# Performance work log

Measured on AMD Instinct MI355X. Metric: run time of the kernel, lower is better.

Reference implementation:

```python
import jax, jax.numpy as jnp
import numpy as np

B, C, W, H = 16, 512, 64, 64
OUT, NH = 512, 8
HD = OUT // NH          # 64
K = 64                  # kernel_size == attended axis length (height)


def setup_inputs() -> dict:
    key = jax.random.key(0)
    k0, k1, k2, k3 = jax.random.split(key, 4)
    s = float(HD) ** -0.5
    return {
        "x": jax.random.normal(k0, (B, C, W, H), jnp.float32),
        "in_proj_weight": jax.random.normal(k1, (2 * OUT, C), jnp.float32) * s,
        "in_proj_bias": jnp.zeros((2 * OUT,), jnp.float32),
        "out_proj_w": jax.random.normal(k2, (OUT, OUT), jnp.float32) * s,
        "out_proj_b": jnp.zeros((OUT,), jnp.float32),
        "relative": jax.random.normal(k3, (2 * HD, 2 * K - 1), jnp.float32) * s,
    }


def reference(x, in_proj_weight, in_proj_bias, out_proj_w, out_proj_b, relative):
    b, c, w, h = x.shape
    hd2 = HD // 2
    # width=False, self-attention path: permute(0,3,2,1) then flat view
    xq = jnp.transpose(x, (0, 3, 2, 1)).reshape(b * w, h, c)
    qkv = xq @ in_proj_weight.T + in_proj_bias
    q, k, v = jnp.split(qkv, [OUT // 2, OUT], axis=2)

    # relative position embeddings gathered into [2*HD, K, K]
    rel_idx = jnp.arange(K)[:, None] - jnp.arange(K)[None, :] + (K - 1)  # key i, query j
    emb = relative[:, rel_idx]                                          # [2*HD, K, K]
    q_emb, k_emb, v_emb = jnp.split(emb, [hd2, HD], axis=0)

    # [bw, heads, ch, pos]
    q = q.reshape(b * w, h, NH, hd2).transpose(0, 2, 3, 1)
    k = k.reshape(b * w, h, NH, hd2).transpose(0, 2, 3, 1)
    v = v.reshape(b * w, h, NH, HD).transpose(0, 2, 3, 1)

    qr = jnp.einsum('bgci,cij->bgij', q, q_emb)
    kr = jnp.einsum('bgci,cij->bgij', k, k_emb).swapaxes(2, 3)
    qk = jnp.einsum('bgci,bgcj->bgij', q, k)
    sim = jax.nn.softmax(qk + qr + kr, axis=3)

    sv = jnp.einsum('bgij,bgcj->bgci', sim, v)     # [bw, NH, HD, h]
    sve = jnp.einsum('bgij,cij->bgci', sim, v_emb)  # [bw, NH, HD, h]
    out = (sv + sve).reshape(b * w, OUT, h).swapaxes(1, 2)  # [bw, h, OUT]
    out = out @ out_proj_w.T + out_proj_b
    # [b, w, h, OUT] -> transpose(2,3) -> permute(0,2,3,1) == transpose(0,3,2,1)
    out = out.reshape(b, w, h, OUT).transpose(0, 3, 2, 1)   # [B, OUT, H, W]
    return out
```

## Files before the change

### kernel.cpp

```cpp
#include <hip/hip_runtime.h>

using u16 = unsigned short;
using u32 = unsigned int;
typedef __attribute__((ext_vector_type(8))) _Float16 h8v;
typedef __attribute__((ext_vector_type(8))) u16 us8;
typedef __attribute__((ext_vector_type(2))) u32 u32x2;
typedef __attribute__((ext_vector_type(4))) float f4v;

__device__ __forceinline__ u16 f2h(float f) {
  _Float16 h = (_Float16)f;
  return __builtin_bit_cast(unsigned short, h);
}
__device__ __forceinline__ _Float16 bits2h(u16 u) {
  return __builtin_bit_cast(_Float16, u);
}

__device__ __forceinline__ f4v mfma16(h8v a, h8v b, f4v c) {
  return __builtin_amdgcn_mfma_f32_16x16x32_f16(a, b, c, 0, 0, 0);
}

__device__ __forceinline__ void gll16(const void* g, void* l) {
  __builtin_amdgcn_global_load_lds(
      (const __attribute__((address_space(1))) void*)g,
      (__attribute__((address_space(3))) void*)l, 16, 0, 0);
}


__global__ __launch_bounds__(256) void k0_setup(
    const float* __restrict__ w1, const float* __restrict__ wout,
    const float* __restrict__ rel, u16* __restrict__ W1b, u16* __restrict__ Woutb,
    u16* __restrict__ EqT, u16* __restrict__ EkT, u16* __restrict__ Evp)
{
  int idx = blockIdx.x * 256 + threadIdx.x;
  if (idx < 524288) {
    W1b[idx] = f2h(w1[idx]);
  } else if (idx < 786432) {
    int k = idx - 524288; Woutb[k] = f2h(wout[k]);
  } else if (idx < 790528) {
    int k = idx - 786432; int t = k >> 5, c = k & 31;
    EqT[k] = (t < 127) ? f2h(rel[c * 127 + t]) : (u16)0;
  } else if (idx < 794624) {
    int k = idx - 790528; int t = k >> 5, c = k & 31;
    EkT[k] = (t < 127) ? f2h(rel[(32 + c) * 127 + t]) : (u16)0;
  } else if (idx < 802816) {
    int k = idx - 794624; int c = k >> 7, t = k & 127;
    Evp[k] = (t < 127) ? f2h(rel[(64 + c) * 127 + t]) : (u16)0;
  }
}

__global__ __launch_bounds__(256) void k0t_transpose(
    const float* __restrict__ x, u16* __restrict__ xT)
{
  const int bid = blockIdx.x;
  const int cc = bid & 7, w = (bid >> 3) & 63, b = bid >> 9;
  const int c0 = cc * 64;
  const int t = threadIdx.x;
  __shared__ float T[64 * 65];

  const float* xb = x + ((size_t)(b * 512 + c0) * 64 + w) * 64;
#pragma unroll
  for (int p = 0; p < 4; p++) {
    int ci = (t >> 4) + p * 16;
    int pos = (t & 15) * 4;
    float4 v = *(const float4*)&xb[(size_t)ci * 4096 + pos];
    T[ci * 65 + pos + 0] = v.x; T[ci * 65 + pos + 1] = v.y;
    T[ci * 65 + pos + 2] = v.z; T[ci * 65 + pos + 3] = v.w;
  }
  __syncthreads();
  size_t Rb = (size_t)b * 4096 + (size_t)w * 64;
#pragma unroll
  for (int p = 0; p < 2; p++) {
    int u = p * 256 + t;
    int h = u >> 3, ch = u & 7;
    us8 o;
#pragma unroll
    for (int e = 0; e < 8; e++) o[e] = f2h(T[(ch * 8 + e) * 65 + h]);
    *(us8*)&xT[(Rb + h) * 512 + c0 + ch * 8] = o;
  }
}

__global__ __launch_bounds__(512, 1) void k1_qkv(
    const u16* __restrict__ xT, const u16* __restrict__ W1b,
    const float* __restrict__ bias, u16* __restrict__ qkv)
{
  __shared__ u16 POOL[81920];
  u16* XL = POOL;
  u16* Bl = POOL + 65536;
  const int rt = blockIdx.x;
  const int b = rt >> 5, w0 = (rt & 31) * 2;
  const int tid = threadIdx.x;
  const int l = tid & 63, wv = tid >> 6;
  const int lr = l & 15, lg = l >> 4;
  const int osub = (wv & 1) * 64;
  const int rsub = (wv >> 1) * 32;
  const size_t Rbase = (size_t)rt * 128;

#pragma unroll
  for (int i = 0; i < 16; i++) {
    int r = wv * 16 + i;
    gll16(xT + (Rbase + r) * 512 + ((l ^ (r & 7)) << 3), XL + r * 512);
  }

  auto stageB = [&](int ot, int kk, int buf) {
#pragma unroll
    for (int q = 0; q < 2; q++) {
      int slot = q * 512 + tid;
      int o = slot >> 3, c4 = slot & 7;
      gll16(W1b + (size_t)(ot * 128 + o) * 512 + kk * 64 + ((c4 ^ (o & 7)) << 3),
            Bl + buf * 8192 + slot * 8);
    }
  };

  stageB(0, 0, 0);
  __syncthreads();

  for (int ot = 0; ot < 8; ot++) {
    const int o0 = ot * 128;
    f4v acc[4][2];
#pragma unroll
    for (int mt = 0; mt < 4; mt++)
#pragma unroll
      for (int nt = 0; nt < 2; nt++) acc[mt][nt] = (f4v){0.f, 0.f, 0.f, 0.f};

#pragma unroll
    for (int kk = 0; kk < 8; kk++) {
      int cur = kk & 1;
      if (kk < 7) stageB(ot, kk + 1, cur ^ 1);
      h8v wf[4][2], xf[2][2];
#pragma unroll
      for (int mt = 0; mt < 4; mt++)
#pragma unroll
        for (int kc = 0; kc < 2; kc++) {
          int o = osub + mt * 16 + lr;
          wf[mt][kc] = *(const h8v*)&Bl[cur * 8192 + o * 64 +
                                        (((kc * 4 + lg) ^ (o & 7)) << 3)];
        }
#pragma unroll
      for (int nt = 0; nt < 2; nt++)
#pragma unroll
        for (int kc = 0; kc < 2; kc++) {
          int r = rsub + nt * 16 + lr;
          xf[nt][kc] = *(const h8v*)&XL[r * 512 + kk * 64 +
                                        (((kc * 4 + lg) ^ (r & 7)) << 3)];
        }
#pragma unroll
      for (int mt = 0; mt < 4; mt++)
#pragma unroll
        for (int nt = 0; nt < 2; nt++)
#pragma unroll
          for (int kc = 0; kc < 2; kc++)
            acc[mt][nt] = mfma16(wf[mt][kc], xf[nt][kc], acc[mt][nt]);
      __syncthreads();
    }

    u16* Tr = Bl;
#pragma unroll
    for (int mt = 0; mt < 4; mt++)
#pragma unroll
      for (int nt = 0; nt < 2; nt++) {
        int r = rsub + nt * 16 + lr;
#pragma unroll
        for (int ep = 0; ep < 2; ep++) {
          int o_ = osub + mt * 16 + lg * 4 + 2 * ep;
          float v0 = acc[mt][nt][2 * ep + 0] + bias[o0 + o_];
          float v1 = acc[mt][nt][2 * ep + 1] + bias[o0 + o_ + 1];
          unsigned pk = (unsigned)f2h(v0) | ((unsigned)f2h(v1) << 16);
          int cc = o_ >> 3;
          int dst = (cc & 8) | ((cc & 7) ^ (r & 7));
          *(unsigned*)&Tr[r * 128 + dst * 8 + (o_ & 7)] = pk;
        }
      }
    __syncthreads();
#pragma unroll
    for (int p = 0; p < 4; p++) {
      int u = p * 512 + tid;
      int r = u >> 4, cc = u & 15;
      int dst = (cc & 8) | ((cc & 7) ^ (r & 7));
      us8 v = *(const us8*)&Tr[r * 128 + dst * 8];
      int h = r & 63, wl = r >> 6;
      size_t S = (size_t)(b * 64 + h) * 64 + w0 + wl;
      *(us8*)&qkv[S * 1024 + o0 + cc * 8] = v;
    }
    __syncthreads();
    if (ot < 7) { stageB(ot + 1, 0, 0); __syncthreads(); }
  }
}

__global__ __launch_bounds__(256) void k2_attn(
    const u16* __restrict__ qkv, const u16* __restrict__ EqT,
    const u16* __restrict__ EkT, const u16* __restrict__ Evp,
    u16* __restrict__ attn)
{
  const int bid = blockIdx.x;
  const int s = bid >> 3, g = bid & 7;
  const int tid = threadIdx.x;
  const int l = tid & 63, wv = tid >> 6;
  const int lr = l & 15, lg = l >> 4;
  const int i0 = wv * 16;
  const u16* base = qkv + (size_t)s * 65536;

  __shared__ __align__(16) u16 POOL[16896];
  u16* QEi = POOL;
  u16* KEj = POOL + 8448;
  u16* Pl  = POOL;
  u16* VTl = POOL + 4096;
  u16* Psh = POOL + 8192;

  us8 vreg0, vreg1;
  {
    int u0 = tid,        j0_ = u0 >> 3, cb0 = u0 & 7;
    int u1 = tid + 256,  j1_ = u1 >> 3, cb1 = u1 & 7;
    vreg0 = *(const us8*)(base + j0_ * 1024 + 512 + g * 64 + cb0 * 8);
    vreg1 = *(const us8*)(base + j1_ * 1024 + 512 + g * 64 + cb1 * 8);
  }

  h8v qf = *(const h8v*)(base + (i0 + lr) * 1024 + g * 32 + lg * 8);
  h8v kf[4];
#pragma unroll
  for (int jt = 0; jt < 4; jt++)
    kf[jt] = *(const h8v*)(base + (jt * 16 + lr) * 1024 + 256 + g * 32 + lg * 8);

  const f4v z4 = {0.f, 0.f, 0.f, 0.f};

#pragma unroll
  for (int tt = 0; tt < 8; tt++) {
    h8v eb = *(const h8v*)(EqT + (tt * 16 + lr) * 32 + lg * 8);
    f4v d = mfma16(eb, qf, z4);
    int tb = tt * 16 + 4 * lg;
    u32x2 pk;
    pk[0] = (u32)f2h(d[0]) | ((u32)f2h(d[1]) << 16);
    pk[1] = (u32)f2h(d[2]) | ((u32)f2h(d[3]) << 16);
    *(u32x2*)&QEi[(i0 + lr) * 132 + tb] = pk;
  }
#pragma unroll
  for (int q = 0; q < 2; q++) {
    int tt = wv * 2 + q;
    h8v ea = *(const h8v*)(EkT + (tt * 16 + lr) * 32 + lg * 8);
#pragma unroll
    for (int jt = 0; jt < 4; jt++) {
      f4v d = mfma16(ea, kf[jt], z4);
      int tb = tt * 16 + 4 * lg;
      u32x2 pk;
      pk[0] = (u32)f2h(d[0]) | ((u32)f2h(d[1]) << 16);
      pk[1] = (u32)f2h(d[2]) | ((u32)f2h(d[3]) << 16);
      *(u32x2*)&KEj[(jt * 16 + lr) * 132 + tb] = pk;
    }
  }
  f4v sc[4];
#pragma unroll
  for (int jt = 0; jt < 4; jt++) sc[jt] = mfma16(kf[jt], qf, z4);

  __syncthreads();

  const int i = i0 + lr;
  float pv[4][4];
  {
    int qbase = i * 133 + 63 - 4 * lg;
    int kbase = 8448 + 4 * lg * 133 + 63 - i;
#pragma unroll
    for (int jt = 0; jt < 4; jt++)
#pragma unroll
      for (int e = 0; e < 4; e++) {
        float qr = (float)bits2h(POOL[qbase - 16 * jt - e]);
        float kr = (float)bits2h(POOL[kbase + 2128 * jt + 133 * e]);
        pv[jt][e] = sc[jt][e] + qr + kr;
      }
  }
  float inv;
  {
    float m = pv[0][0];
#pragma unroll
    for (int jt = 0; jt < 4; jt++)
#pragma unroll
      for (int e = 0; e < 4; e++) m = fmaxf(m, pv[jt][e]);
    m = fmaxf(m, __shfl_xor(m, 16));
    m = fmaxf(m, __shfl_xor(m, 32));
    float t0 = 0.f;
#pragma unroll
    for (int jt = 0; jt < 4; jt++)
#pragma unroll
      for (int e = 0; e < 4; e++) {
        pv[jt][e] = exp2f((pv[jt][e] - m) * 1.4426950408889634f);
        t0 += pv[jt][e];
      }
    t0 += __shfl_xor(t0, 16);
    t0 += __shfl_xor(t0, 32);
    inv = 1.f / t0;
  }
#pragma unroll
  for (int jt = 0; jt < 4; jt++)
#pragma unroll
    for (int e = 0; e < 4; e++) pv[jt][e] *= inv;

  __syncthreads();

#pragma unroll
  for (int jt = 0; jt < 4; jt++) {
    int j0 = jt * 16 + 4 * lg;
    int jc = j0 >> 3;
    u32x2 pk;
    pk[0] = (u32)f2h(pv[jt][0]) | ((u32)f2h(pv[jt][1]) << 16);
    pk[1] = (u32)f2h(pv[jt][2]) | ((u32)f2h(pv[jt][3]) << 16);
    *(u32x2*)&Pl[i * 64 + ((jc ^ (i & 7)) << 3) + (j0 & 7)] = pk;
#pragma unroll
    for (int e = 0; e < 4; e++) {
      int d = i + 63 - (j0 + e);
      int cd = d >> 3;
      Psh[i * 128 + (((cd & 8) | ((cd & 7) ^ (i & 7))) << 3) + (d & 7)] =
          f2h(pv[jt][e]);
    }
  }
  {
    int zi = tid >> 2;
#pragma unroll
    for (int kk = 0; kk < 16; kk++) {
      int k = (tid & 3) * 16 + kk;
      int col = (k < zi) ? k : (k + 64);
      int cd = col >> 3;
      Psh[zi * 128 + (((cd & 8) | ((cd & 7) ^ (zi & 7))) << 3) + (col & 7)] = 0;
    }
    int u0 = tid, j0_ = u0 >> 3, cb0 = u0 & 7;
#pragma unroll
    for (int e = 0; e < 8; e++) {
      int c = cb0 * 8 + e;
      VTl[c * 64 + (((j0_ >> 3) ^ (c & 7)) << 3) + (j0_ & 7)] = (u16)vreg0[e];
    }
    int u1 = tid + 256, j1_ = u1 >> 3, cb1 = u1 & 7;
#pragma unroll
    for (int e = 0; e < 8; e++) {
      int c = cb1 * 8 + e;
      VTl[c * 64 + (((j1_ >> 3) ^ (c & 7)) << 3) + (j1_ & 7)] = (u16)vreg1[e];
    }
  }
  __syncthreads();

  f4v acc[4] = {z4, z4, z4, z4};
  {
#pragma unroll
    for (int kc = 0; kc < 2; kc++) {
      h8v pa = *(const h8v*)&Pl[i * 64 + (((kc * 4 + lg) ^ (i & 7)) << 3)];
#pragma unroll
      for (int ct = 0; ct < 4; ct++) {
        int cA = ct * 16 + lr;
        h8v vb = *(const h8v*)&VTl[cA * 64 + (((kc * 4 + lg) ^ (cA & 7)) << 3)];
        acc[ct] = mfma16(pa, vb, acc[ct]);
      }
    }
#pragma unroll
    for (int tc = 0; tc < 4; tc++) {
      int cd = tc * 4 + lg;
      int cds = (cd & 8) | ((cd & 7) ^ (i & 7));
      h8v pa = *(const h8v*)&Psh[i * 128 + cds * 8];
#pragma unroll
      for (int ct = 0; ct < 4; ct++) {
        h8v eb = *(const h8v*)(Evp + (ct * 16 + lr) * 128 + tc * 32 + lg * 8);
        acc[ct] = mfma16(pa, eb, acc[ct]);
      }
    }
  }
#pragma unroll
  for (int ct = 0; ct < 4; ct++)
#pragma unroll
    for (int r = 0; r < 4; r++) {
      int io = i0 + lg * 4 + r;
      attn[(size_t)(s * 64 + io) * 512 + g * 64 + ct * 16 + lr] = f2h(acc[ct][r]);
    }
}

__global__ __launch_bounds__(512) void k3_oproj(
    const u16* __restrict__ attn, const u16* __restrict__ Woutb,
    const float* __restrict__ ob, float* __restrict__ out)
{
  const int bid = blockIdx.x;
  const int b = bid >> 6, w = bid & 63;
  const int tid = threadIdx.x;
  const int l = tid & 63, wv = tid >> 6;
  const int lr = l & 15, lg = l >> 4;

  __shared__ u16 Bl[2][64 * 64];

  f4v acc[4][4];
#pragma unroll
  for (int a_ = 0; a_ < 4; a_++)
#pragma unroll
    for (int b_ = 0; b_ < 4; b_++) acc[a_][b_] = (f4v){0.f, 0.f, 0.f, 0.f};

  auto stageB = [&](int kk, int buf) {
    int c0 = kk * 64;
    int h_l = wv * 8 + (l >> 3);
    int p = l & 7;
    const u16* src = attn + ((size_t)b * 4096 + (size_t)h_l * 64 + w) * 512 + c0 +
                     ((p ^ (h_l & 7)) << 3);
    gll16(src, &Bl[buf][wv * 512]);
  };

  stageB(0, 0);
  __syncthreads();

  for (int kk = 0; kk < 8; kk++) {
    int cur = kk & 1, nxt = cur ^ 1;
    if (kk < 7) stageB(kk + 1, nxt);
    int c0 = kk * 64;
    h8v af[4][2], bf[4][2];
#pragma unroll
    for (int mt = 0; mt < 4; mt++)
#pragma unroll
      for (int kc = 0; kc < 2; kc++)
        af[mt][kc] = *(const h8v*)(Woutb + (size_t)(wv * 64 + mt * 16 + lr) * 512 +
                                   c0 + kc * 32 + lg * 8);
#pragma unroll
    for (int jt = 0; jt < 4; jt++)
#pragma unroll
      for (int kc = 0; kc < 2; kc++) {
        int h = jt * 16 + lr;
        bf[jt][kc] = *(const h8v*)&Bl[cur][h * 64 + (((kc * 4 + lg) ^ (h & 7)) << 3)];
      }
#pragma unroll
    for (int mt = 0; mt < 4; mt++)
#pragma unroll
      for (int jt = 0; jt < 4; jt++)
#pragma unroll
        for (int kc = 0; kc < 2; kc++)
          acc[mt][jt] = mfma16(af[mt][kc], bf[jt][kc], acc[mt][jt]);
    __syncthreads();
  }

#pragma unroll
  for (int mt = 0; mt < 4; mt++)
#pragma unroll
    for (int jt = 0; jt < 4; jt++)
#pragma unroll
      for (int e = 0; e < 4; e++) {
        int o = wv * 64 + mt * 16 + lg * 4 + e;
        int h = jt * 16 + lr;
        out[(((size_t)b * 512 + o) * 64 + w) * 64 + h] = acc[mt][jt][e] + ob[o];
      }
}

extern "C" void kernel_launch(void* const* d_in, const int* in_sizes, int n_in,
                              void* d_out, int out_size, void* d_ws, size_t ws_size,
                              hipStream_t stream)
{
  (void)in_sizes; (void)n_in; (void)out_size; (void)ws_size;
  const float* x    = (const float*)d_in[0];
  const float* w1   = (const float*)d_in[1];
  const float* b1   = (const float*)d_in[2];
  const float* wout = (const float*)d_in[3];
  const float* bo   = (const float*)d_in[4];
  const float* rel  = (const float*)d_in[5];
  float* out = (float*)d_out;

  char* ws = (char*)d_ws;
  u16* qkv_ws  = (u16*)ws;
  u16* attn_ws = (u16*)(ws + 134217728);
  u16* xT_ws   = attn_ws;
  u16* W1b     = (u16*)(ws + 201326592);
  u16* Woutb   = (u16*)(ws + 202375168);
  u16* EqT     = (u16*)(ws + 202899456);
  u16* EkT     = (u16*)(ws + 202907648);
  u16* Evp     = (u16*)(ws + 202915840);

  k0_setup<<<dim3(3136), dim3(256), 0, stream>>>(w1, wout, rel, W1b, Woutb, EqT, EkT, Evp);
  k0t_transpose<<<dim3(8192), dim3(256), 0, stream>>>(x, xT_ws);
  k1_qkv  <<<dim3(512),  dim3(512), 0, stream>>>(xT_ws, W1b, b1, qkv_ws);
  k2_attn <<<dim3(8192), dim3(256), 0, stream>>>(qkv_ws, EqT, EkT, Evp, attn_ws);
  k3_oproj<<<dim3(1024), dim3(512), 0, stream>>>(attn_ws, Woutb, bo, out);
}
```

Before: 337.9 us.

## Halve QKV projection tile to 64 rows with 256-thread blocks and two blocks per CU

```diff
diff --git a/kernel.cpp b/kernel.cpp
--- a/kernel.cpp
+++ b/kernel.cpp
@@ -79,21 +79,21 @@
   }
 }
 
-__global__ __launch_bounds__(512, 1) void k1_qkv(
+__global__ __launch_bounds__(256, 2) void k1_qkv(
     const u16* __restrict__ xT, const u16* __restrict__ W1b,
     const float* __restrict__ bias, u16* __restrict__ qkv)
 {
-  __shared__ u16 POOL[81920];
+  __shared__ u16 POOL[40960];
   u16* XL = POOL;
-  u16* Bl = POOL + 65536;
-  const int rt = blockIdx.x;
-  const int b = rt >> 5, w0 = (rt & 31) * 2;
+  u16* WD = POOL + 32768;
+  const int bid = blockIdx.x;
+  const int b = bid >> 6, w = bid & 63;
   const int tid = threadIdx.x;
   const int l = tid & 63, wv = tid >> 6;
   const int lr = l & 15, lg = l >> 4;
   const int osub = (wv & 1) * 64;
   const int rsub = (wv >> 1) * 32;
-  const size_t Rbase = (size_t)rt * 128;
+  const size_t Rbase = (size_t)bid * 64;
 
 #pragma unroll
   for (int i = 0; i < 16; i++) {
@@ -104,10 +104,11 @@
   auto stageB = [&](int ot, int kk, int buf) {
 #pragma unroll
     for (int q = 0; q < 2; q++) {
-      int slot = q * 512 + tid;
-      int o = slot >> 3, c4 = slot & 7;
-      gll16(W1b + (size_t)(ot * 128 + o) * 512 + kk * 64 + ((c4 ^ (o & 7)) << 3),
-            Bl + buf * 8192 + slot * 8);
+      int slot = q * 256 + tid;
+      int o = slot >> 2, c4 = slot & 3;
+      gll16(W1b + (size_t)(ot * 128 + o) * 512 + kk * 32 +
+                ((c4 ^ ((o >> 1) & 3)) << 3),
+            WD + buf * 4096 + slot * 8);
     }
   };
 
@@ -123,47 +124,45 @@
       for (int nt = 0; nt < 2; nt++) acc[mt][nt] = (f4v){0.f, 0.f, 0.f, 0.f};
 
 #pragma unroll
-    for (int kk = 0; kk < 8; kk++) {
+    for (int kk = 0; kk < 16; kk++) {
       int cur = kk & 1;
-      if (kk < 7) stageB(ot, kk + 1, cur ^ 1);
-      h8v wf[4][2], xf[2][2];
-#pragma unroll
-      for (int mt = 0; mt < 4; mt++)
-#pragma unroll
-        for (int kc = 0; kc < 2; kc++) {
-          int o = osub + mt * 16 + lr;
-          wf[mt][kc] = *(const h8v*)&Bl[cur * 8192 + o * 64 +
-                                        (((kc * 4 + lg) ^ (o & 7)) << 3)];
-        }
-#pragma unroll
-      for (int nt = 0; nt < 2; nt++)
-#pragma unroll
-        for (int kc = 0; kc < 2; kc++) {
-          int r = rsub + nt * 16 + lr;
-          xf[nt][kc] = *(const h8v*)&XL[r * 512 + kk * 64 +
-                                        (((kc * 4 + lg) ^ (r & 7)) << 3)];
-        }
-#pragma unroll
-      for (int mt = 0; mt < 4; mt++)
-#pragma unroll
-        for (int nt = 0; nt < 2; nt++)
-#pragma unroll
-          for (int kc = 0; kc < 2; kc++)
-            acc[mt][nt] = mfma16(wf[mt][kc], xf[nt][kc], acc[mt][nt]);
-      __syncthreads();
-    }
-
-    u16* Tr = Bl;
-#pragma unroll
-    for (int mt = 0; mt < 4; mt++)
+      if (kk < 15) stageB(ot, kk + 1, cur ^ 1);
+      h8v wf[4], xf[2];
+#pragma unroll
+      for (int mt = 0; mt < 4; mt++) {
+        int o = osub + mt * 16 + lr;
+        wf[mt] = *(const h8v*)&WD[cur * 4096 + o * 32 +
+                                  ((lg ^ ((o >> 1) & 3)) << 3)];
+      }
 #pragma unroll
       for (int nt = 0; nt < 2; nt++) {
         int r = rsub + nt * 16 + lr;
+        int cc = kk * 4 + lg;
+        xf[nt] = *(const h8v*)&XL[r * 512 + ((cc ^ (r & 7)) << 3)];
+      }
+#pragma unroll
+      for (int mt = 0; mt < 4; mt++)
+#pragma unroll
+        for (int nt = 0; nt < 2; nt++)
+          acc[mt][nt] = mfma16(wf[mt], xf[nt], acc[mt][nt]);
+      __syncthreads();
+    }
+
+    u16* Tr = WD;
+    float4 bias4[4];
+#pragma unroll
+    for (int mt = 0; mt < 4; mt++)
+      bias4[mt] = *(const float4*)&bias[o0 + osub + mt * 16 + lg * 4];
+#pragma unroll
+    for (int mt = 0; mt < 4; mt++)
+#pragma unroll
+      for (int nt = 0; nt < 2; nt++) {
+        int r = rsub + nt * 16 + lr;
 #pragma unroll
         for (int ep = 0; ep < 2; ep++) {
           int o_ = osub + mt * 16 + lg * 4 + 2 * ep;
-          float v0 = acc[mt][nt][2 * ep + 0] + bias[o0 + o_];
-          float v1 = acc[mt][nt][2 * ep + 1] + bias[o0 + o_ + 1];
+          float v0 = acc[mt][nt][2 * ep + 0] + ((const float*)&bias4[mt])[2 * ep + 0];
+          float v1 = acc[mt][nt][2 * ep + 1] + ((const float*)&bias4[mt])[2 * ep + 1];
           unsigned pk = (unsigned)f2h(v0) | ((unsigned)f2h(v1) << 16);
           int cc = o_ >> 3;
           int dst = (cc & 8) | ((cc & 7) ^ (r & 7));
@@ -173,12 +172,11 @@
     __syncthreads();
 #pragma unroll
     for (int p = 0; p < 4; p++) {
-      int u = p * 512 + tid;
+      int u = p * 256 + tid;
       int r = u >> 4, cc = u & 15;
       int dst = (cc & 8) | ((cc & 7) ^ (r & 7));
       us8 v = *(const us8*)&Tr[r * 128 + dst * 8];
-      int h = r & 63, wl = r >> 6;
-      size_t S = (size_t)(b * 64 + h) * 64 + w0 + wl;
+      size_t S = (size_t)(b * 64 + r) * 64 + w;
       *(us8*)&qkv[S * 1024 + o0 + cc * 8] = v;
     }
     __syncthreads();
@@ -462,7 +460,7 @@
 
   k0_setup<<<dim3(3136), dim3(256), 0, stream>>>(w1, wout, rel, W1b, Woutb, EqT, EkT, Evp);
   k0t_transpose<<<dim3(8192), dim3(256), 0, stream>>>(x, xT_ws);
-  k1_qkv  <<<dim3(512),  dim3(512), 0, stream>>>(xT_ws, W1b, b1, qkv_ws);
+  k1_qkv  <<<dim3(1024), dim3(256), 0, stream>>>(xT_ws, W1b, b1, qkv_ws);
   k2_attn <<<dim3(8192), dim3(256), 0, stream>>>(qkv_ws, EqT, EkT, Evp, attn_ws);
   k3_oproj<<<dim3(1024), dim3(512), 0, stream>>>(attn_ws, Woutb, bo, out);
 }
```

Measured after the change: 341.8 us. No clear change (+1.2%).
